# Performance work log

Measured on AMD Instinct MI355X. Metric: run time of the kernel, lower is better.

## Reference

```python
import jax, jax.numpy as jnp
import numpy as np
from jax import lax

D_MODEL = 2048
D_INNER = 4096  # expand * d_model
D_CONV = 4
B, T = 4, 2048


def _rmsnorm(h):
    # F.normalize(x, dim=-1) * sqrt(D): x / max(||x||_2, 1e-12) * sqrt(D)
    n = jnp.sqrt(jnp.sum(h * h, axis=-1, keepdims=True))
    return h / jnp.maximum(n, 1e-12) * (h.shape[-1] ** 0.5)


def setup_inputs() -> dict:
    key = jax.random.key(0)
    ks = jax.random.split(key, 7)
    std = 0.02
    return {
        "x": jax.random.normal(ks[0], (B, T, D_MODEL), jnp.float32),
        "W_in": jax.random.normal(ks[1], (2 * D_INNER, D_MODEL), jnp.float32) * std,
        "conv_w": jax.random.normal(ks[2], (D_INNER, 1, D_CONV), jnp.float32) * std,
        "conv_b": jnp.zeros((D_INNER,), jnp.float32),
        "W_out": jax.random.normal(ks[3], (D_MODEL, D_INNER), jnp.float32) * std,
        "W_mlp1": jax.random.normal(ks[4], (4 * D_MODEL, D_MODEL), jnp.float32) * std,
        "W_mlp2": jax.random.normal(ks[5], (D_MODEL, 4 * D_MODEL), jnp.float32) * std,
    }


def _mamba_fallback(h, W_in, conv_w, conv_b, W_out):
    # in_proj: (B,T,D) -> (B,T,2*d_inner), split into x branch and gate z
    xz = jnp.einsum("btd,ed->bte", h, W_in)
    xp, z = jnp.split(xz, 2, axis=-1)
    # depthwise causal conv over time: torch pads (d_conv-1) both sides then slices [:T]
    # == left-pad-only causal cross-correlation
    xc = lax.conv_general_dilated(
        xp.transpose(0, 2, 1),  # (B, d_inner, T)
        conv_w,                  # (d_inner, 1, d_conv)
        window_strides=(1,),
        padding=[(D_CONV - 1, 0)],
        dimension_numbers=("NCH", "OIH", "NCH"),
        feature_group_count=D_INNER,
    ) + conv_b[None, :, None]
    xc = xc.transpose(0, 2, 1)  # (B, T, d_inner)
    y = jax.nn.silu(xc) * jax.nn.silu(z)
    return jnp.einsum("bte,de->btd", y, W_out)


def reference(x, W_in, conv_w, conv_b, W_out, W_mlp1, W_mlp2):
    # full-dimension path (active_dim=None)
    h = _rmsnorm(x)
    x = x + _mamba_fallback(h, W_in, conv_w, conv_b, W_out)
    h = _rmsnorm(x)
    m = jnp.einsum("bte,de->btd", jax.nn.relu(jnp.einsum("btd,ed->bte", h, W_mlp1)), W_mlp2)
    return x + m
```

## Files before the change

kernel.cpp:

```cpp
#include <hip/hip_runtime.h>
#include <hip/hip_bf16.h>

typedef __bf16 bf16;
typedef __bf16 bf16x8 __attribute__((ext_vector_type(8)));
typedef float f32x4 __attribute__((ext_vector_type(4)));

#define D_MODEL 2048
#define D_INNER 4096
#define ROWS    8192

__device__ __forceinline__ void gload_lds16(const void* g, void* l) {
    __builtin_amdgcn_global_load_lds(
        (const __attribute__((address_space(1))) void*)g,
        (__attribute__((address_space(3))) void*)l, 16, 0, 0);
}

__global__ __launch_bounds__(256) void f2b_kernel(const float* __restrict__ in,
                                                  bf16* __restrict__ out, int n8) {
    int i = blockIdx.x * 256 + threadIdx.x;
    if (i >= n8) return;
    long base = (long)i * 8;
    float4 a = *(const float4*)(in + base);
    float4 b = *(const float4*)(in + base + 4);
    bf16x8 o;
    o[0] = (bf16)a.x; o[1] = (bf16)a.y; o[2] = (bf16)a.z; o[3] = (bf16)a.w;
    o[4] = (bf16)b.x; o[5] = (bf16)b.y; o[6] = (bf16)b.z; o[7] = (bf16)b.w;
    *(bf16x8*)(out + base) = o;
}

__global__ __launch_bounds__(256) void rmsnorm_kernel(const float* __restrict__ x,
                                                      bf16* __restrict__ h) {
    const long row = blockIdx.x;
    const float* xr = x + row * D_MODEL;
    float4 v0 = ((const float4*)xr)[threadIdx.x * 2];
    float4 v1 = ((const float4*)xr)[threadIdx.x * 2 + 1];
    float ss = v0.x*v0.x + v0.y*v0.y + v0.z*v0.z + v0.w*v0.w
             + v1.x*v1.x + v1.y*v1.y + v1.z*v1.z + v1.w*v1.w;
    #pragma unroll
    for (int o = 32; o; o >>= 1) ss += __shfl_xor(ss, o, 64);
    __shared__ float red[4];
    if ((threadIdx.x & 63) == 0) red[threadIdx.x >> 6] = ss;
    __syncthreads();
    float tot = red[0] + red[1] + red[2] + red[3];
    float scale = 45.254834f / fmaxf(sqrtf(tot), 1e-12f);
    bf16x8 o;
    o[0] = (bf16)(v0.x*scale); o[1] = (bf16)(v0.y*scale);
    o[2] = (bf16)(v0.z*scale); o[3] = (bf16)(v0.w*scale);
    o[4] = (bf16)(v1.x*scale); o[5] = (bf16)(v1.y*scale);
    o[6] = (bf16)(v1.z*scale); o[7] = (bf16)(v1.w*scale);
    *(bf16x8*)(h + row * D_MODEL + threadIdx.x * 8) = o;
}

__global__ __launch_bounds__(256) void conv_gate_kernel(bf16* __restrict__ xz,
                                                        const float* __restrict__ cw,
                                                        const float* __restrict__ cb) {
    const int idx = blockIdx.x * 256 + threadIdx.x;
    const int c8  = idx & 511;
    const int row = idx >> 9;
    const int t   = row & 2047;
    const int c0  = c8 * 8;
    float acc[8];
    float wv[8][4];
    #pragma unroll
    for (int e = 0; e < 8; ++e) {
        float4 f = ((const float4*)cw)[c0 + e];
        wv[e][0] = f.x; wv[e][1] = f.y; wv[e][2] = f.z; wv[e][3] = f.w;
        acc[e] = cb[c0 + e];
    }
    #pragma unroll
    for (int j = 0; j < 4; ++j) {
        if (t + j - 3 >= 0) {
            bf16x8 xv = *(const bf16x8*)(xz + (long)(row + j - 3) * (2*D_INNER) + c0);
            #pragma unroll
            for (int e = 0; e < 8; ++e) acc[e] += (float)xv[e] * wv[e][j];
        }
    }
    bf16* zp = xz + (long)row * (2*D_INNER) + D_INNER + c0;
    bf16x8 zv = *(const bf16x8*)zp;
    bf16x8 yv;
    #pragma unroll
    for (int e = 0; e < 8; ++e) {
        float xc = acc[e];
        float s1 = xc / (1.f + __expf(-xc));
        float z  = (float)zv[e];
        float s2 = z / (1.f + __expf(-z));
        yv[e] = (bf16)(s1 * s2);
    }
    *(bf16x8*)zp = yv;
}

template<int EPI>
__global__ __launch_bounds__(512, 2) void gemm_bt(
        const bf16* __restrict__ A, long lda,
        const bf16* __restrict__ B,
        void* __restrict__ C, const float* __restrict__ res,
        int N, int K, int gx) {
    __shared__ __align__(16) char LB[131072];
    const int tid = threadIdx.x;
    const int w   = tid >> 6;
    const int l   = tid & 63;
    const int lr  = l & 15;

    const int nwg = gridDim.x;
    const int qq  = nwg >> 3;
    const int sw  = (blockIdx.x & 7) * qq + (blockIdx.x >> 3);
    const int bx  = sw % gx, by = sw / gx;
    const long rowBase = (long)by * 256;
    const long colBase = (long)bx * 256;

    const int srow = w * 8 + (l >> 3);
    const int schk = (l & 7) ^ ((l >> 3) & 7);
    const bf16* aSrc = A + (rowBase + srow) * lda + schk * 8;
    const bf16* bSrc = B + (colBase + srow) * (long)K + schk * 8;
    const long lda64 = 64 * lda;
    const long ldb64 = 64 * (long)K;
    const int  w1024 = w * 1024;

    auto stgA = [&](int DBB, int kt) {
        const bf16* s = aSrc + (long)kt * 64;
        gload_lds16(s,            LB + DBB +     0 + w1024);
        gload_lds16(s +   lda64,  LB + DBB +  8192 + w1024);
        gload_lds16(s + 2*lda64,  LB + DBB + 16384 + w1024);
        gload_lds16(s + 3*lda64,  LB + DBB + 24576 + w1024);
    };
    auto stgB = [&](int DBB, int kt) {
        const bf16* s = bSrc + (long)kt * 64;
        gload_lds16(s,            LB + DBB + 32768 + w1024);
        gload_lds16(s +   ldb64,  LB + DBB + 40960 + w1024);
        gload_lds16(s + 2*ldb64,  LB + DBB + 49152 + w1024);
        gload_lds16(s + 3*ldb64,  LB + DBB + 57344 + w1024);
    };

    const int cx0 = (((l >> 4)    ) ^ (l & 7)) << 4;
    const int cx1 = (((l >> 4) + 4) ^ (l & 7)) << 4;
    const int hm = w >> 2;
    const int q  = w & 3;
    int aRow[8], bRow[4];
    #pragma unroll
    for (int m = 0; m < 8; ++m) aRow[m] = hm * 16384 + (m * 16 + lr) * 128;
    #pragma unroll
    for (int n = 0; n < 4; ++n)
        bRow[n] = 32768 + (q >> 1) * 16384 + ((q & 1) * 64 + n * 16 + lr) * 128;

    const int nt  = K >> 6;
    const int nit = nt >> 1;
    f32x4 acc[8][4] = {};
    bf16x8 AX[4][2], BL[2][2], BH[2][2];

    stgB(0, 0);      stgA(0, 0);
    stgB(65536, 1);  stgA(65536, 1);
    asm volatile("s_waitcnt vmcnt(8)" ::: "memory");
    __builtin_amdgcn_s_barrier();
    __builtin_amdgcn_sched_barrier(0);
    #pragma unroll
    for (int m = 0; m < 4; ++m) {
        AX[m][0] = *(const bf16x8*)(LB + aRow[m] + cx0);
        AX[m][1] = *(const bf16x8*)(LB + aRow[m] + cx1);
    }
    #pragma unroll
    for (int n = 0; n < 2; ++n) {
        BL[n][0] = *(const bf16x8*)(LB + bRow[n]     + cx0);
        BL[n][1] = *(const bf16x8*)(LB + bRow[n]     + cx1);
    }
    #pragma unroll
    for (int n = 0; n < 2; ++n) {
        BH[n][0] = *(const bf16x8*)(LB + bRow[n + 2] + cx0);
        BH[n][1] = *(const bf16x8*)(LB + bRow[n + 2] + cx1);
    }
    asm volatile("s_waitcnt lgkmcnt(4)" ::: "memory");
    __builtin_amdgcn_sched_barrier(0);
    __builtin_amdgcn_s_setprio(1);
    #pragma unroll
    for (int m = 0; m < 4; ++m)
        #pragma unroll
        for (int n = 0; n < 2; ++n) {
            acc[m][n] = __builtin_amdgcn_mfma_f32_16x16x32_bf16(AX[m][0], BL[n][0], acc[m][n], 0, 0, 0);
            acc[m][n] = __builtin_amdgcn_mfma_f32_16x16x32_bf16(AX[m][1], BL[n][1], acc[m][n], 0, 0, 0);
        }
    __builtin_amdgcn_s_setprio(0);
    __builtin_amdgcn_s_barrier();

    for (int it = 0; it < nit; ++it) {
        int kA = 2 * it + 2; if (kA >= nt) kA = 0;
        int kB = 2 * it + 3; if (kB >= nt) kB = 0;
        #pragma unroll
        for (int db = 0; db < 2; ++db) {
            const int DBB = db * 65536;
            const char* Lb = LB + DBB;
            const char* Ln = LB + (DBB ^ 65536);
            const int kst = db ? kB : kA;
            const bool full = (db == 0) || (it < nit - 1);

            stgB(DBB, kst);
            __builtin_amdgcn_s_setprio(1);
            #pragma unroll
            for (int m = 0; m < 4; ++m)
                #pragma unroll
                for (int n = 0; n < 2; ++n) {
                    acc[m][n + 2] = __builtin_amdgcn_mfma_f32_16x16x32_bf16(AX[m][0], BH[n][0], acc[m][n + 2], 0, 0, 0);
                    acc[m][n + 2] = __builtin_amdgcn_mfma_f32_16x16x32_bf16(AX[m][1], BH[n][1], acc[m][n + 2], 0, 0, 0);
                }
            __builtin_amdgcn_s_setprio(0);
            asm volatile("s_waitcnt vmcnt(4)" ::: "memory");
            __builtin_amdgcn_sched_barrier(0);
            #pragma unroll
            for (int m = 0; m < 4; ++m) {
                AX[m][0] = *(const bf16x8*)(Lb + aRow[m + 4] + cx0);
                AX[m][1] = *(const bf16x8*)(Lb + aRow[m + 4] + cx1);
            }
            asm volatile("s_waitcnt lgkmcnt(0)" ::: "memory");
            __builtin_amdgcn_sched_barrier(0);
            __builtin_amdgcn_s_setprio(1);
            #pragma unroll
            for (int m = 0; m < 4; ++m)
                #pragma unroll
                for (int n = 0; n < 2; ++n) {
                    acc[m + 4][n + 2] = __builtin_amdgcn_mfma_f32_16x16x32_bf16(AX[m][0], BH[n][0], acc[m + 4][n + 2], 0, 0, 0);
                    acc[m + 4][n + 2] = __builtin_amdgcn_mfma_f32_16x16x32_bf16(AX[m][1], BH[n][1], acc[m + 4][n + 2], 0, 0, 0);
                }
            __builtin_amdgcn_s_setprio(0);
            __builtin_amdgcn_s_barrier();

            __builtin_amdgcn_s_setprio(1);
            #pragma unroll
            for (int m = 0; m < 4; ++m)
                #pragma unroll
                for (int n = 0; n < 2; ++n) {
                    acc[m + 4][n] = __builtin_amdgcn_mfma_f32_16x16x32_bf16(AX[m][0], BL[n][0], acc[m + 4][n], 0, 0, 0);
                    acc[m + 4][n] = __builtin_amdgcn_mfma_f32_16x16x32_bf16(AX[m][1], BL[n][1], acc[m + 4][n], 0, 0, 0);
                }
            __builtin_amdgcn_s_setprio(0);
            __builtin_amdgcn_sched_barrier(0);
            stgA(DBB, kst);
            if (full) {
                #pragma unroll
                for (int m = 0; m < 4; ++m) {
                    AX[m][0] = *(const bf16x8*)(Ln + aRow[m] + cx0);
                    AX[m][1] = *(const bf16x8*)(Ln + aRow[m] + cx1);
                }
                #pragma unroll
                for (int n = 0; n < 2; ++n) {
                    BL[n][0] = *(const bf16x8*)(Ln + bRow[n]     + cx0);
                    BL[n][1] = *(const bf16x8*)(Ln + bRow[n]     + cx1);
                }
                #pragma unroll
                for (int n = 0; n < 2; ++n) {
                    BH[n][0] = *(const bf16x8*)(Ln + bRow[n + 2] + cx0);
                    BH[n][1] = *(const bf16x8*)(Ln + bRow[n + 2] + cx1);
                }
                asm volatile("s_waitcnt lgkmcnt(4)" ::: "memory");
                __builtin_amdgcn_sched_barrier(0);
                __builtin_amdgcn_s_setprio(1);
                #pragma unroll
                for (int m = 0; m < 4; ++m)
                    #pragma unroll
                    for (int n = 0; n < 2; ++n) {
                        acc[m][n] = __builtin_amdgcn_mfma_f32_16x16x32_bf16(AX[m][0], BL[n][0], acc[m][n], 0, 0, 0);
                        acc[m][n] = __builtin_amdgcn_mfma_f32_16x16x32_bf16(AX[m][1], BL[n][1], acc[m][n], 0, 0, 0);
                    }
                __builtin_amdgcn_s_setprio(0);
            }
            __builtin_amdgcn_s_barrier();
        }
    }

    asm volatile("s_waitcnt vmcnt(0)" ::: "memory");
    __builtin_amdgcn_s_barrier();

    const int lg = l >> 4;
    const long wrow = rowBase + hm * 128;
    const long wcol = colBase + q * 64;
    char* ep = LB + w * 16384;

    if (EPI == 2) {
        #pragma unroll
        for (int mh = 0; mh < 2; ++mh) {
            #pragma unroll
            for (int m = 0; m < 4; ++m) {
                #pragma unroll
                for (int n = 0; n < 4; ++n) {
                    f32x4 v = acc[mh * 4 + m][n];
                    #pragma unroll
                    for (int r = 0; r < 4; ++r) {
                        int rowr = m * 16 + lg * 4 + r;
                        int chnk = (n * 4 + (lr >> 2)) ^ (rowr & 7);
                        *(float*)(ep + rowr * 256 + chnk * 16 + (lr & 3) * 4) = v[r];
                    }
                }
            }
            asm volatile("s_waitcnt lgkmcnt(0)" ::: "memory");
            #pragma unroll
            for (int i = 0; i < 16; ++i) {
                int rr = i * 4 + (l >> 4);
                float4 lv = *(float4*)(ep + rr * 256 + (((l & 15) ^ (rr & 7)) * 16));
                long off = (wrow + mh * 64 + rr) * N + wcol + (l & 15) * 4;
                float4 rv = *(const float4*)(res + off);
                lv.x += rv.x; lv.y += rv.y; lv.z += rv.z; lv.w += rv.w;
                *(float4*)((float*)C + off) = lv;
            }
            if (mh == 0) { asm volatile("s_waitcnt lgkmcnt(0) vmcnt(0)" ::: "memory"); }
        }
    } else {
        #pragma unroll
        for (int m = 0; m < 8; ++m) {
            #pragma unroll
            for (int n = 0; n < 4; ++n) {
                f32x4 v = acc[m][n];
                #pragma unroll
                for (int r = 0; r < 4; ++r) {
                    int rowr = m * 16 + lg * 4 + r;
                    int chnk = (n * 2 + (lr >> 3)) ^ (rowr & 7);
                    float val = (EPI == 1) ? fmaxf(v[r], 0.f) : v[r];
                    *(bf16*)(ep + rowr * 128 + chnk * 16 + (lr & 7) * 2) = (bf16)val;
                }
            }
        }
        asm volatile("s_waitcnt lgkmcnt(0)" ::: "memory");
        #pragma unroll
        for (int i = 0; i < 16; ++i) {
            int rr = i * 8 + (l >> 3);
            uint4 lv = *(uint4*)(ep + rr * 128 + (((l & 7) ^ (rr & 7)) * 16));
            *(uint4*)((bf16*)C + (wrow + rr) * N + wcol + (l & 7) * 8) = lv;
        }
    }
}

extern "C" void kernel_launch(void* const* d_in, const int* in_sizes, int n_in,
                              void* d_out, int out_size, void* d_ws, size_t ws_size,
                              hipStream_t stream) {
    const float* x      = (const float*)d_in[0];
    const float* W_in   = (const float*)d_in[1];
    const float* cw     = (const float*)d_in[2];
    const float* cb     = (const float*)d_in[3];
    const float* W_out  = (const float*)d_in[4];
    const float* W_mlp1 = (const float*)d_in[5];
    const float* W_mlp2 = (const float*)d_in[6];
    float* out = (float*)d_out;

    char* ws  = (char*)d_ws;
    bf16* wW  = (bf16*)(ws);
    bf16* h   = (bf16*)(ws + 33554432);
    bf16* xz  = (bf16*)(ws + 67108864);
    float* x2 = (float*)(ws + 201326592);
    bf16* y   = xz + D_INNER;
    bf16* m1  = xz;

    dim3 blk(256);
    dim3 gblk(512);

    f2b_kernel<<<dim3(8192), blk, 0, stream>>>(W_in, wW, 16777216/8);
    rmsnorm_kernel<<<dim3(ROWS), blk, 0, stream>>>(x, h);
    gemm_bt<0><<<dim3(1024), gblk, 0, stream>>>(h, D_MODEL, wW, xz, nullptr, 2*D_INNER, D_MODEL, 32);
    conv_gate_kernel<<<dim3(16384), blk, 0, stream>>>(xz, cw, cb);
    f2b_kernel<<<dim3(4096), blk, 0, stream>>>(W_out, wW, 8388608/8);
    gemm_bt<2><<<dim3(256), gblk, 0, stream>>>(y, 2*D_INNER, wW, x2, x, D_MODEL, D_INNER, 8);

    rmsnorm_kernel<<<dim3(ROWS), blk, 0, stream>>>(x2, h);
    f2b_kernel<<<dim3(8192), blk, 0, stream>>>(W_mlp1, wW, 16777216/8);
    gemm_bt<1><<<dim3(1024), gblk, 0, stream>>>(h, D_MODEL, wW, m1, nullptr, 4*D_MODEL, D_MODEL, 32);
    f2b_kernel<<<dim3(8192), blk, 0, stream>>>(W_mlp2, wW, 16777216/8);
    gemm_bt<2><<<dim3(256), gblk, 0, stream>>>(m1, 4*D_MODEL, wW, out, x2, D_MODEL, 4*D_MODEL, 8);
}
```

Baseline: 1.003 ms.

## Double-buffer GEMM register fragments to overlap LDS reads with MFMA

Splits the A fragment registers into two sets and double-buffers B fragments by K-stage. This lets the second half of A and the next stage's operands be read from LDS while MFMAs on the current fragments run. The goal is to hide LDS read latency behind matrix-core work. It raises VGPR pressure, which could lower occupancy or cause spills, and it moves the barrier and wait placement in the pipelined loop.

```diff
diff --git a/kernel.cpp b/kernel.cpp
--- a/kernel.cpp
+++ b/kernel.cpp
@@ -145,7 +145,7 @@
     const int nt  = K >> 6;
     const int nit = nt >> 1;
     f32x4 acc[8][4] = {};
-    bf16x8 AX[4][2], BL[2][2], BH[2][2];
+    bf16x8 FA0[4][2], FA1[4][2], BLs[2][2][2], BHs[2][2][2];
 
     stgB(0, 0);      stgA(0, 0);
     stgB(65536, 1);  stgA(65536, 1);
@@ -154,18 +154,18 @@
     __builtin_amdgcn_sched_barrier(0);
     #pragma unroll
     for (int m = 0; m < 4; ++m) {
-        AX[m][0] = *(const bf16x8*)(LB + aRow[m] + cx0);
-        AX[m][1] = *(const bf16x8*)(LB + aRow[m] + cx1);
+        FA0[m][0] = *(const bf16x8*)(LB + aRow[m] + cx0);
+        FA0[m][1] = *(const bf16x8*)(LB + aRow[m] + cx1);
     }
     #pragma unroll
     for (int n = 0; n < 2; ++n) {
-        BL[n][0] = *(const bf16x8*)(LB + bRow[n]     + cx0);
-        BL[n][1] = *(const bf16x8*)(LB + bRow[n]     + cx1);
+        BLs[0][n][0] = *(const bf16x8*)(LB + bRow[n]     + cx0);
+        BLs[0][n][1] = *(const bf16x8*)(LB + bRow[n]     + cx1);
     }
     #pragma unroll
     for (int n = 0; n < 2; ++n) {
-        BH[n][0] = *(const bf16x8*)(LB + bRow[n + 2] + cx0);
-        BH[n][1] = *(const bf16x8*)(LB + bRow[n + 2] + cx1);
+        BHs[0][n][0] = *(const bf16x8*)(LB + bRow[n + 2] + cx0);
+        BHs[0][n][1] = *(const bf16x8*)(LB + bRow[n + 2] + cx1);
     }
     asm volatile("s_waitcnt lgkmcnt(4)" ::: "memory");
     __builtin_amdgcn_sched_barrier(0);
@@ -174,8 +174,8 @@
     for (int m = 0; m < 4; ++m)
         #pragma unroll
         for (int n = 0; n < 2; ++n) {
-            acc[m][n] = __builtin_amdgcn_mfma_f32_16x16x32_bf16(AX[m][0], BL[n][0], acc[m][n], 0, 0, 0);
-            acc[m][n] = __builtin_amdgcn_mfma_f32_16x16x32_bf16(AX[m][1], BL[n][1], acc[m][n], 0, 0, 0);
+            acc[m][n] = __builtin_amdgcn_mfma_f32_16x16x32_bf16(FA0[m][0], BLs[0][n][0], acc[m][n], 0, 0, 0);
+            acc[m][n] = __builtin_amdgcn_mfma_f32_16x16x32_bf16(FA0[m][1], BLs[0][n][1], acc[m][n], 0, 0, 0);
         }
     __builtin_amdgcn_s_setprio(0);
     __builtin_amdgcn_s_barrier();
@@ -185,69 +185,76 @@
         int kB = 2 * it + 3; if (kB >= nt) kB = 0;
         #pragma unroll
         for (int db = 0; db < 2; ++db) {
+            const int cs = db;
+            const int ns = db ^ 1;
             const int DBB = db * 65536;
             const char* Lb = LB + DBB;
             const char* Ln = LB + (DBB ^ 65536);
             const int kst = db ? kB : kA;
             const bool full = (db == 0) || (it < nit - 1);
 
+            asm volatile("s_waitcnt lgkmcnt(0)" ::: "memory");
+            __builtin_amdgcn_sched_barrier(0);
+            #pragma unroll
+            for (int m = 0; m < 4; ++m) {
+                FA1[m][0] = *(const bf16x8*)(Lb + aRow[m + 4] + cx0);
+                FA1[m][1] = *(const bf16x8*)(Lb + aRow[m + 4] + cx1);
+            }
+            __builtin_amdgcn_sched_barrier(0);
             stgB(DBB, kst);
             __builtin_amdgcn_s_setprio(1);
             #pragma unroll
             for (int m = 0; m < 4; ++m)
                 #pragma unroll
                 for (int n = 0; n < 2; ++n) {
-                    acc[m][n + 2] = __builtin_amdgcn_mfma_f32_16x16x32_bf16(AX[m][0], BH[n][0], acc[m][n + 2], 0, 0, 0);
-                    acc[m][n + 2] = __builtin_amdgcn_mfma_f32_16x16x32_bf16(AX[m][1], BH[n][1], acc[m][n + 2], 0, 0, 0);
+                    acc[m][n + 2] = __builtin_amdgcn_mfma_f32_16x16x32_bf16(FA0[m][0], BHs[cs][n][0], acc[m][n + 2], 0, 0, 0);
+                    acc[m][n + 2] = __builtin_amdgcn_mfma_f32_16x16x32_bf16(FA0[m][1], BHs[cs][n][1], acc[m][n + 2], 0, 0, 0);
+                }
+            __builtin_amdgcn_s_setprio(0);
+            asm volatile("s_waitcnt lgkmcnt(0)" ::: "memory");
+            __builtin_amdgcn_sched_barrier(0);
+            __builtin_amdgcn_s_setprio(1);
+            #pragma unroll
+            for (int m = 0; m < 4; ++m)
+                #pragma unroll
+                for (int n = 0; n < 2; ++n) {
+                    acc[m + 4][n + 2] = __builtin_amdgcn_mfma_f32_16x16x32_bf16(FA1[m][0], BHs[cs][n][0], acc[m + 4][n + 2], 0, 0, 0);
+                    acc[m + 4][n + 2] = __builtin_amdgcn_mfma_f32_16x16x32_bf16(FA1[m][1], BHs[cs][n][1], acc[m + 4][n + 2], 0, 0, 0);
                 }
             __builtin_amdgcn_s_setprio(0);
             asm volatile("s_waitcnt vmcnt(4)" ::: "memory");
-            __builtin_amdgcn_sched_barrier(0);
-            #pragma unroll
-            for (int m = 0; m < 4; ++m) {
-                AX[m][0] = *(const bf16x8*)(Lb + aRow[m + 4] + cx0);
-                AX[m][1] = *(const bf16x8*)(Lb + aRow[m + 4] + cx1);
-            }
-            asm volatile("s_waitcnt lgkmcnt(0)" ::: "memory");
-            __builtin_amdgcn_sched_barrier(0);
+            __builtin_amdgcn_s_barrier();
+            __builtin_amdgcn_sched_barrier(0);
+
+            if (full) {
+                #pragma unroll
+                for (int m = 0; m < 4; ++m) {
+                    FA0[m][0] = *(const bf16x8*)(Ln + aRow[m] + cx0);
+                    FA0[m][1] = *(const bf16x8*)(Ln + aRow[m] + cx1);
+                }
+                #pragma unroll
+                for (int n = 0; n < 2; ++n) {
+                    BLs[ns][n][0] = *(const bf16x8*)(Ln + bRow[n]     + cx0);
+                    BLs[ns][n][1] = *(const bf16x8*)(Ln + bRow[n]     + cx1);
+                }
+                #pragma unroll
+                for (int n = 0; n < 2; ++n) {
+                    BHs[ns][n][0] = *(const bf16x8*)(Ln + bRow[n + 2] + cx0);
+                    BHs[ns][n][1] = *(const bf16x8*)(Ln + bRow[n + 2] + cx1);
+                }
+                __builtin_amdgcn_sched_barrier(0);
+            }
+            stgA(DBB, kst);
             __builtin_amdgcn_s_setprio(1);
             #pragma unroll
             for (int m = 0; m < 4; ++m)
                 #pragma unroll
                 for (int n = 0; n < 2; ++n) {
-                    acc[m + 4][n + 2] = __builtin_amdgcn_mfma_f32_16x16x32_bf16(AX[m][0], BH[n][0], acc[m + 4][n + 2], 0, 0, 0);
-                    acc[m + 4][n + 2] = __builtin_amdgcn_mfma_f32_16x16x32_bf16(AX[m][1], BH[n][1], acc[m + 4][n + 2], 0, 0, 0);
+                    acc[m + 4][n] = __builtin_amdgcn_mfma_f32_16x16x32_bf16(FA1[m][0], BLs[cs][n][0], acc[m + 4][n], 0, 0, 0);
+                    acc[m + 4][n] = __builtin_amdgcn_mfma_f32_16x16x32_bf16(FA1[m][1], BLs[cs][n][1], acc[m + 4][n], 0, 0, 0);
                 }
             __builtin_amdgcn_s_setprio(0);
-            __builtin_amdgcn_s_barrier();
-
-            __builtin_amdgcn_s_setprio(1);
-            #pragma unroll
-            for (int m = 0; m < 4; ++m)
-                #pragma unroll
-                for (int n = 0; n < 2; ++n) {
-                    acc[m + 4][n] = __builtin_amdgcn_mfma_f32_16x16x32_bf16(AX[m][0], BL[n][0], acc[m + 4][n], 0, 0, 0);
-                    acc[m + 4][n] = __builtin_amdgcn_mfma_f32_16x16x32_bf16(AX[m][1], BL[n][1], acc[m + 4][n], 0, 0, 0);
-                }
-            __builtin_amdgcn_s_setprio(0);
-            __builtin_amdgcn_sched_barrier(0);
-            stgA(DBB, kst);
             if (full) {
-                #pragma unroll
-                for (int m = 0; m < 4; ++m) {
-                    AX[m][0] = *(const bf16x8*)(Ln + aRow[m] + cx0);
-                    AX[m][1] = *(const bf16x8*)(Ln + aRow[m] + cx1);
-                }
-                #pragma unroll
-                for (int n = 0; n < 2; ++n) {
-                    BL[n][0] = *(const bf16x8*)(Ln + bRow[n]     + cx0);
-                    BL[n][1] = *(const bf16x8*)(Ln + bRow[n]     + cx1);
-                }
-                #pragma unroll
-                for (int n = 0; n < 2; ++n) {
-                    BH[n][0] = *(const bf16x8*)(Ln + bRow[n + 2] + cx0);
-                    BH[n][1] = *(const bf16x8*)(Ln + bRow[n + 2] + cx1);
-                }
                 asm volatile("s_waitcnt lgkmcnt(4)" ::: "memory");
                 __builtin_amdgcn_sched_barrier(0);
                 __builtin_amdgcn_s_setprio(1);
@@ -255,12 +262,13 @@
                 for (int m = 0; m < 4; ++m)
                     #pragma unroll
                     for (int n = 0; n < 2; ++n) {
-                        acc[m][n] = __builtin_amdgcn_mfma_f32_16x16x32_bf16(AX[m][0], BL[n][0], acc[m][n], 0, 0, 0);
-                        acc[m][n] = __builtin_amdgcn_mfma_f32_16x16x32_bf16(AX[m][1], BL[n][1], acc[m][n], 0, 0, 0);
+                        acc[m][n] = __builtin_amdgcn_mfma_f32_16x16x32_bf16(FA0[m][0], BLs[ns][n][0], acc[m][n], 0, 0, 0);
+                        acc[m][n] = __builtin_amdgcn_mfma_f32_16x16x32_bf16(FA0[m][1], BLs[ns][n][1], acc[m][n], 0, 0, 0);
                     }
                 __builtin_amdgcn_s_setprio(0);
             }
             __builtin_amdgcn_s_barrier();
+            __builtin_amdgcn_sched_barrier(0);
         }
     }
 
```

New measurement: 3.601 ms. 259% more time.

## Add 4-wave 256x256 GEMM kernel with 128x128 per-wave tiles for wide projections

Applied to the files above, without the earlier changes.

Adds a new GEMM kernel that uses 256 threads (4 waves), each computing a 128x128 sub-tile with 64 MFMA accumulators. It double-buffers 64-wide K slices in LDS and splits each slice's register loads into two halves that are interleaved with MFMA work. The epilogue stages bf16 results through swizzled LDS before writing them out. It replaces the 512-thread kernel for the in_proj and MLP1 GEMMs, aiming for more reuse per wave and less LDS traffic. The cost is very high register pressure and only one workgroup per CU.

```diff
diff --git a/kernel.cpp b/kernel.cpp
--- a/kernel.cpp
+++ b/kernel.cpp
@@ -87,6 +87,135 @@
         yv[e] = (bf16)(s1 * s2);
     }
     *(bf16x8*)zp = yv;
+}
+
+template<int EPI>
+__global__ __launch_bounds__(256, 1) void gemm_w4(
+        const bf16* __restrict__ A, long lda,
+        const bf16* __restrict__ B,
+        bf16* __restrict__ C,
+        int N, int K, int gx) {
+    __shared__ __align__(16) char LB[131072];
+    const int tid = threadIdx.x;
+    const int w   = tid >> 6;
+    const int l   = tid & 63;
+    const int lr  = l & 15;
+
+    const int nwg = gridDim.x;
+    const int qq  = nwg >> 3;
+    const int sw  = (blockIdx.x & 7) * qq + (blockIdx.x >> 3);
+    const int bx  = sw % gx, by = sw / gx;
+    const long rowBase = (long)by * 256;
+    const long colBase = (long)bx * 256;
+
+    const int srow = tid >> 3;
+    const int schk = (tid & 7) ^ ((tid >> 3) & 7);
+    const bf16* aSrc = A + (rowBase + srow) * lda + schk * 8;
+    const bf16* bSrc = B + (colBase + srow) * (long)K + schk * 8;
+    const int w1024 = w * 1024;
+
+    auto stg = [&](int DBB, int kt) {
+        const bf16* sa = aSrc + (long)kt * 64;
+        const bf16* sb = bSrc + (long)kt * 64;
+        #pragma unroll
+        for (int i = 0; i < 8; ++i)
+            gload_lds16(sa + (long)(32 * i) * lda, LB + DBB + i * 4096 + w1024);
+        #pragma unroll
+        for (int i = 0; i < 8; ++i)
+            gload_lds16(sb + (long)(32 * i) * (long)K, LB + DBB + 32768 + i * 4096 + w1024);
+    };
+
+    const int wr = (w >> 1) * 128;
+    const int wc = (w & 1) * 128;
+    const int cx0 = (((l >> 4)    ) ^ (l & 7)) << 4;
+    const int cx1 = (((l >> 4) + 4) ^ (l & 7)) << 4;
+    int aRow[8], bRow[8];
+    #pragma unroll
+    for (int m = 0; m < 8; ++m) aRow[m] = (wr + m * 16 + lr) * 128;
+    #pragma unroll
+    for (int n = 0; n < 8; ++n) bRow[n] = 32768 + (wc + n * 16 + lr) * 128;
+
+    const int nt = K >> 6;
+    f32x4 acc[8][8] = {};
+    bf16x8 a0[8], b0[8], a1[8], b1[8];
+
+    stg(0, 0);
+    stg(65536, 1);
+    asm volatile("s_waitcnt vmcnt(16)" ::: "memory");
+    __builtin_amdgcn_s_barrier();
+    __builtin_amdgcn_sched_barrier(0);
+    #pragma unroll
+    for (int m = 0; m < 8; ++m) a0[m] = *(const bf16x8*)(LB + aRow[m] + cx0);
+    #pragma unroll
+    for (int n = 0; n < 8; ++n) b0[n] = *(const bf16x8*)(LB + bRow[n] + cx0);
+
+    for (int t = 0; t < nt; ++t) {
+        const char* Lb = (const char*)LB + ((t & 1) << 16);
+        int kst = t + 2; if (kst >= nt) kst = 0;
+
+        #pragma unroll
+        for (int m = 0; m < 8; ++m) a1[m] = *(const bf16x8*)(Lb + aRow[m] + cx1);
+        asm volatile("s_waitcnt lgkmcnt(8)" ::: "memory");
+        __builtin_amdgcn_sched_barrier(0);
+        #pragma unroll
+        for (int n = 0; n < 8; ++n) b1[n] = *(const bf16x8*)(Lb + bRow[n] + cx1);
+        __builtin_amdgcn_sched_barrier(0);
+        __builtin_amdgcn_s_setprio(1);
+        #pragma unroll
+        for (int m = 0; m < 8; ++m)
+            #pragma unroll
+            for (int n = 0; n < 8; ++n)
+                acc[m][n] = __builtin_amdgcn_mfma_f32_16x16x32_bf16(a0[m], b0[n], acc[m][n], 0, 0, 0);
+        __builtin_amdgcn_s_setprio(0);
+        asm volatile("s_waitcnt lgkmcnt(0)" ::: "memory");
+        __builtin_amdgcn_sched_barrier(0);
+        stg((t & 1) << 16, kst);
+        __builtin_amdgcn_s_setprio(1);
+        #pragma unroll
+        for (int m = 0; m < 8; ++m)
+            #pragma unroll
+            for (int n = 0; n < 8; ++n)
+                acc[m][n] = __builtin_amdgcn_mfma_f32_16x16x32_bf16(a1[m], b1[n], acc[m][n], 0, 0, 0);
+        __builtin_amdgcn_s_setprio(0);
+        asm volatile("s_waitcnt vmcnt(16)" ::: "memory");
+        __builtin_amdgcn_s_barrier();
+        __builtin_amdgcn_sched_barrier(0);
+        if (t + 1 < nt) {
+            const char* Ln = (const char*)LB + (((t + 1) & 1) << 16);
+            #pragma unroll
+            for (int m = 0; m < 8; ++m) a0[m] = *(const bf16x8*)(Ln + aRow[m] + cx0);
+            #pragma unroll
+            for (int n = 0; n < 8; ++n) b0[n] = *(const bf16x8*)(Ln + bRow[n] + cx0);
+        }
+    }
+
+    asm volatile("s_waitcnt vmcnt(0)" ::: "memory");
+    __builtin_amdgcn_s_barrier();
+
+    const int lg = l >> 4;
+    char* ep = LB + w * 32768;
+    #pragma unroll
+    for (int m = 0; m < 8; ++m) {
+        #pragma unroll
+        for (int n = 0; n < 8; ++n) {
+            f32x4 v = acc[m][n];
+            #pragma unroll
+            for (int r = 0; r < 4; ++r) {
+                int rowr = m * 16 + lg * 4 + r;
+                int chnk = (n * 2 + (lr >> 3)) ^ (rowr & 7);
+                float val = (EPI == 1) ? fmaxf(v[r], 0.f) : v[r];
+                *(bf16*)(ep + rowr * 256 + chnk * 16 + (lr & 7) * 2) = (bf16)val;
+            }
+        }
+    }
+    asm volatile("s_waitcnt lgkmcnt(0)" ::: "memory");
+    #pragma unroll
+    for (int i = 0; i < 32; ++i) {
+        int rr = i * 4 + (l >> 4);
+        int lc = l & 15;
+        uint4 lv = *(uint4*)(ep + rr * 256 + ((lc ^ (rr & 7)) * 16));
+        *(uint4*)(C + (rowBase + wr + rr) * N + colBase + wc + lc * 8) = lv;
+    }
 }
 
 template<int EPI>
@@ -350,14 +479,14 @@
 
     f2b_kernel<<<dim3(8192), blk, 0, stream>>>(W_in, wW, 16777216/8);
     rmsnorm_kernel<<<dim3(ROWS), blk, 0, stream>>>(x, h);
-    gemm_bt<0><<<dim3(1024), gblk, 0, stream>>>(h, D_MODEL, wW, xz, nullptr, 2*D_INNER, D_MODEL, 32);
+    gemm_w4<0><<<dim3(1024), blk, 0, stream>>>(h, D_MODEL, wW, xz, 2*D_INNER, D_MODEL, 32);
     conv_gate_kernel<<<dim3(16384), blk, 0, stream>>>(xz, cw, cb);
     f2b_kernel<<<dim3(4096), blk, 0, stream>>>(W_out, wW, 8388608/8);
     gemm_bt<2><<<dim3(256), gblk, 0, stream>>>(y, 2*D_INNER, wW, x2, x, D_MODEL, D_INNER, 8);
 
     rmsnorm_kernel<<<dim3(ROWS), blk, 0, stream>>>(x2, h);
     f2b_kernel<<<dim3(8192), blk, 0, stream>>>(W_mlp1, wW, 16777216/8);
-    gemm_bt<1><<<dim3(1024), gblk, 0, stream>>>(h, D_MODEL, wW, m1, nullptr, 4*D_MODEL, D_MODEL, 32);
+    gemm_w4<1><<<dim3(1024), blk, 0, stream>>>(h, D_MODEL, wW, m1, 4*D_MODEL, D_MODEL, 32);
     f2b_kernel<<<dim3(8192), blk, 0, stream>>>(W_mlp2, wW, 16777216/8);
     gemm_bt<2><<<dim3(256), gblk, 0, stream>>>(m1, 4*D_MODEL, wW, out, x2, D_MODEL, 4*D_MODEL, 8);
 }
```

Result: slower. 1.160 ms (+15.7%).

## Merge elementwise prep kernels and remap GEMM tiles per XCD

Applied to the files above, without the earlier changes.

Combines rmsnorm with the weight fp32-to-bf16 conversion, and conv-gate with the W_out conversion, into single launches. Blocks are split by index, so independent memory-bound work runs concurrently and there are fewer launches and tail bubbles. The 32-column-tile GEMMs also get a new block-to-tile mapping that gives each XCD a contiguous 8x16 tile region, improving L2 reuse of A and B. The merged kernels may branch inside a block only if the grids are misaligned, but the grid split here is block-aligned.

```diff
diff --git a/kernel.cpp b/kernel.cpp
--- a/kernel.cpp
+++ b/kernel.cpp
@@ -15,9 +15,8 @@
         (__attribute__((address_space(3))) void*)l, 16, 0, 0);
 }
 
-__global__ __launch_bounds__(256) void f2b_kernel(const float* __restrict__ in,
-                                                  bf16* __restrict__ out, int n8) {
-    int i = blockIdx.x * 256 + threadIdx.x;
+__device__ __forceinline__ void f2b_body(const float* __restrict__ in,
+                                         bf16* __restrict__ out, int i, int n8) {
     if (i >= n8) return;
     long base = (long)i * 8;
     float4 a = *(const float4*)(in + base);
@@ -28,10 +27,9 @@
     *(bf16x8*)(out + base) = o;
 }
 
-__global__ __launch_bounds__(256) void rmsnorm_kernel(const float* __restrict__ x,
-                                                      bf16* __restrict__ h) {
-    const long row = blockIdx.x;
-    const float* xr = x + row * D_MODEL;
+__device__ __forceinline__ void rmsnorm_body(const float* __restrict__ x,
+                                             bf16* __restrict__ h, int row) {
+    const float* xr = x + (long)row * D_MODEL;
     float4 v0 = ((const float4*)xr)[threadIdx.x * 2];
     float4 v1 = ((const float4*)xr)[threadIdx.x * 2 + 1];
     float ss = v0.x*v0.x + v0.y*v0.y + v0.z*v0.z + v0.w*v0.w
@@ -48,13 +46,12 @@
     o[2] = (bf16)(v0.z*scale); o[3] = (bf16)(v0.w*scale);
     o[4] = (bf16)(v1.x*scale); o[5] = (bf16)(v1.y*scale);
     o[6] = (bf16)(v1.z*scale); o[7] = (bf16)(v1.w*scale);
-    *(bf16x8*)(h + row * D_MODEL + threadIdx.x * 8) = o;
-}
-
-__global__ __launch_bounds__(256) void conv_gate_kernel(bf16* __restrict__ xz,
-                                                        const float* __restrict__ cw,
-                                                        const float* __restrict__ cb) {
-    const int idx = blockIdx.x * 256 + threadIdx.x;
+    *(bf16x8*)(h + (long)row * D_MODEL + threadIdx.x * 8) = o;
+}
+
+__device__ __forceinline__ void conv_body(bf16* __restrict__ xz,
+                                          const float* __restrict__ cw,
+                                          const float* __restrict__ cb, int idx) {
     const int c8  = idx & 511;
     const int row = idx >> 9;
     const int t   = row & 2047;
@@ -87,6 +84,28 @@
         yv[e] = (bf16)(s1 * s2);
     }
     *(bf16x8*)zp = yv;
+}
+
+__global__ __launch_bounds__(256) void prep_kernel(const float* __restrict__ x,
+                                                   bf16* __restrict__ h,
+                                                   const float* __restrict__ w,
+                                                   bf16* __restrict__ wOut, int n8) {
+    if ((int)blockIdx.x < ROWS) rmsnorm_body(x, h, blockIdx.x);
+    else f2b_body(w, wOut, (blockIdx.x - ROWS) * 256 + threadIdx.x, n8);
+}
+
+__global__ __launch_bounds__(256) void convf2b_kernel(bf16* __restrict__ xz,
+                                                      const float* __restrict__ cw,
+                                                      const float* __restrict__ cb,
+                                                      const float* __restrict__ w,
+                                                      bf16* __restrict__ wOut, int n8) {
+    if ((int)blockIdx.x < 16384) conv_body(xz, cw, cb, blockIdx.x * 256 + threadIdx.x);
+    else f2b_body(w, wOut, (blockIdx.x - 16384) * 256 + threadIdx.x, n8);
+}
+
+__global__ __launch_bounds__(256) void f2b_kernel(const float* __restrict__ in,
+                                                  bf16* __restrict__ out, int n8) {
+    f2b_body(in, out, blockIdx.x * 256 + threadIdx.x, n8);
 }
 
 template<int EPI>
@@ -101,10 +120,16 @@
     const int l   = tid & 63;
     const int lr  = l & 15;
 
-    const int nwg = gridDim.x;
-    const int qq  = nwg >> 3;
-    const int sw  = (blockIdx.x & 7) * qq + (blockIdx.x >> 3);
-    const int bx  = sw % gx, by = sw / gx;
+    int bx, by;
+    if (gx == 32) {
+        const int xcd = blockIdx.x & 7, i = blockIdx.x >> 3;
+        by = (xcd >> 1) * 8 + (i >> 4);
+        bx = (xcd & 1) * 16 + (i & 15);
+    } else {
+        const int qq = gridDim.x >> 3;
+        const int sw = (blockIdx.x & 7) * qq + (blockIdx.x >> 3);
+        bx = sw % gx; by = sw / gx;
+    }
     const long rowBase = (long)by * 256;
     const long colBase = (long)bx * 256;
 
@@ -348,15 +373,12 @@
     dim3 blk(256);
     dim3 gblk(512);
 
-    f2b_kernel<<<dim3(8192), blk, 0, stream>>>(W_in, wW, 16777216/8);
-    rmsnorm_kernel<<<dim3(ROWS), blk, 0, stream>>>(x, h);
+    prep_kernel<<<dim3(ROWS + 8192), blk, 0, stream>>>(x, h, W_in, wW, 16777216/8);
     gemm_bt<0><<<dim3(1024), gblk, 0, stream>>>(h, D_MODEL, wW, xz, nullptr, 2*D_INNER, D_MODEL, 32);
-    conv_gate_kernel<<<dim3(16384), blk, 0, stream>>>(xz, cw, cb);
-    f2b_kernel<<<dim3(4096), blk, 0, stream>>>(W_out, wW, 8388608/8);
+    convf2b_kernel<<<dim3(16384 + 4096), blk, 0, stream>>>(xz, cw, cb, W_out, wW, 8388608/8);
     gemm_bt<2><<<dim3(256), gblk, 0, stream>>>(y, 2*D_INNER, wW, x2, x, D_MODEL, D_INNER, 8);
 
-    rmsnorm_kernel<<<dim3(ROWS), blk, 0, stream>>>(x2, h);
-    f2b_kernel<<<dim3(8192), blk, 0, stream>>>(W_mlp1, wW, 16777216/8);
+    prep_kernel<<<dim3(ROWS + 8192), blk, 0, stream>>>(x2, h, W_mlp1, wW, 16777216/8);
     gemm_bt<1><<<dim3(1024), gblk, 0, stream>>>(h, D_MODEL, wW, m1, nullptr, 4*D_MODEL, D_MODEL, 32);
     f2b_kernel<<<dim3(8192), blk, 0, stream>>>(W_mlp2, wW, 16777216/8);
     gemm_bt<2><<<dim3(256), gblk, 0, stream>>>(m1, 4*D_MODEL, wW, out, x2, D_MODEL, 4*D_MODEL, 8);
```

Measured after the change: 961.4 us. 1.04x faster.
